# Performance work log

Measured on AMD Instinct MI355X. Metric: run time of the kernel, lower is better.

Reference implementation:

```python
import jax, jax.numpy as jnp
import numpy as np

# Grid / camera constants (from repo config and hardcoded module values)
D = 256                 # FRUSTUM3D.GRID_DIMENSIONS = [256,256,256]
TRUNC = 3.0             # FRUSTUM3D.TRUNCATION (densify default for geometry)
VOX = 0.03              # voxel size (points *= 0.03)
H, W = 240, 320         # rendered image size (from plot_image ticks)
FX = FY = 240.0
CX, CY = 160.0, 120.0
CENTER = jnp.array([3.825, 3.825, 3.825], dtype=jnp.float32)
OFFSETS = jnp.array([[0.0, 0.0, 0.0], [0.8, 0.0, 0.15], [0.75, 0.0, 0.1], [-0.85, 0.0, 0.1]], dtype=jnp.float32)
ANGLES = jnp.array([0.0, 0.0, 0.3, 2.15], dtype=jnp.float32)
N_PTS = 2_000_000


def setup_inputs() -> dict:
    key = jax.random.key(0)
    k1, k2, k3, k4 = jax.random.split(key, 4)
    # unique voxel coordinates (sparse tensor coords are unique by construction)
    flat = jax.random.permutation(k1, D * D * D)[:N_PTS]
    ix = flat // (D * D)
    iy = (flat // D) % D
    iz = flat % D
    geo_coords = jnp.stack([ix, iy, iz], axis=1).astype(jnp.int32)
    geo_feats = (jax.random.uniform(k2, (N_PTS,)) * 2.0).astype(jnp.float32)  # ~half < 1.0 -> surface
    rgb_feats = jax.random.uniform(k3, (N_PTS, 3), dtype=jnp.float32)
    aux_views = jax.random.uniform(k4, (1, 4, 3, H, W), dtype=jnp.float32)
    # valid SE(3) poses: identity rotation, camera at z = -6 looking toward the volume
    T = np.eye(4, dtype=np.float32)
    T[2, 3] = -6.0
    cam_poses = jnp.asarray(np.stack([T] * 4)[None])  # [1,4,4,4]
    return {"geo_coords": geo_coords, "geo_feats": geo_feats, "rgb_feats": rgb_feats,
            "aux_views": aux_views, "cam_poses": cam_poses}


def _rot_y(a):
    ca, sa = jnp.cos(a), jnp.sin(a)
    return jnp.array([[ca, 0.0, sa], [0.0, 1.0, 0.0], [-sa, 0.0, ca]], dtype=jnp.float32)


def reference(geo_coords, geo_feats, rgb_feats, aux_views, cam_poses):
    ix, iy, iz = geo_coords[:, 0], geo_coords[:, 1], geo_coords[:, 2]
    # sparse -> dense densify (geometry default = truncation, rgb default = 0)
    dense_geo = jnp.full((D, D, D), TRUNC, dtype=geo_feats.dtype).at[ix, iy, iz].set(geo_feats)
    dense_rgb = jnp.zeros((D, D, D, 3), dtype=rgb_feats.dtype).at[ix, iy, iz].set(rgb_feats)
    # surface extraction: geometry < 1.0 (non-set voxels have value TRUNC >= 1 -> never surface,
    # so surface voxels are exactly the input coords with feat < 1; fixed-shape masked form)
    surf = dense_geo[ix, iy, iz] < 1.0                      # [N]
    pts_rgb = dense_rgb[ix, iy, iz]                         # [N,3]  (= rgb[:, surface_mask].T)
    points = geo_coords.astype(jnp.float32) * VOX - CENTER  # [N,3]

    def render(T, offset, angle):
        R = T[:3, :3] @ _rot_y(angle)
        c = T[:3, 3] + offset
        pc = (points - c) @ R                               # camera-frame points, [N,3]
        z = pc[:, 2]
        vis = surf & (z > 1e-4)
        zs = jnp.where(vis, z, 1.0)
        u = jnp.round(FX * pc[:, 0] / zs + CX).astype(jnp.int32)
        v = jnp.round(FY * pc[:, 1] / zs + CY).astype(jnp.int32)
        inb = vis & (u >= 0) & (u < W) & (v >= 0) & (v < H)
        flat = jnp.where(inb, v * W + u, H * W)             # H*W -> dropped
        depth = jnp.where(inb, z, jnp.inf)
        zbuf = jnp.full(H * W, jnp.inf, dtype=jnp.float32).at[flat].min(depth, mode='drop')
        win = inb & (depth <= zbuf[jnp.clip(flat, 0, H * W - 1)])
        wf = win.astype(pts_rgb.dtype)
        num = jnp.zeros((H * W, 3), dtype=pts_rgb.dtype).at[flat].add(pts_rgb * wf[:, None], mode='drop')
        cnt = jnp.zeros((H * W,), dtype=pts_rgb.dtype).at[flat].add(wf, mode='drop')
        return (num / jnp.maximum(cnt, 1.0)[:, None]).reshape(H, W, 3)

    imgs = jax.vmap(render)(cam_poses[0], OFFSETS, ANGLES)          # [4,H,W,3]
    views = jnp.transpose(aux_views[0], (0, 2, 3, 1))               # [4,H,W,3]
    mask = (imgs != 0.0).astype(imgs.dtype)                         # elementwise, like torch.where(img==0,0,1)
    n = 3.0 * jnp.sum(mask, axis=(1, 2, 3))                         # per-view N
    l = jnp.sum(jnp.abs(imgs * mask - views * mask), axis=(1, 2, 3))
    return jnp.sum(jnp.where(n > 0, l / jnp.maximum(n, 1.0), 0.0))
```

## Files before the change

kernel.cpp:

```cpp
#include <hip/hip_runtime.h>

#define HWPIX (240 * 320)
#define VWORDS (4 * HWPIX)
#define NBINS 960
#define NB 256
#define CAP 3000000

__device__ __forceinline__ float dot3(float a0, float b0, float a1, float b1,
                                      float a2, float b2) {
  return __fadd_rn(__fadd_rn(__fmul_rn(a0, b0), __fmul_rn(a1, b1)),
                   __fmul_rn(a2, b2));
}

__device__ __forceinline__ bool project(const float* __restrict__ P, float px,
                                        float py, float pz, int& u, int& v,
                                        unsigned& zb) {
  float dx = __fsub_rn(px, P[9]);
  float dy = __fsub_rn(py, P[10]);
  float dz = __fsub_rn(pz, P[11]);
  float z = dot3(dx, P[2], dy, P[5], dz, P[8]);
  if (!(z > 1e-4f)) return false;
  float x = dot3(dx, P[0], dy, P[3], dz, P[6]);
  float y = dot3(dx, P[1], dy, P[4], dz, P[7]);
  u = (int)rintf(__fadd_rn(__fdiv_rn(__fmul_rn(240.0f, x), z), 160.0f));
  v = (int)rintf(__fadd_rn(__fdiv_rn(__fmul_rn(240.0f, y), z), 120.0f));
  if (u < 0 || u >= 320 || v < 0 || v >= 240) return false;
  zb = __float_as_uint(z);
  return true;
}

__global__ void k_init(const float* __restrict__ cam, float* __restrict__ params,
                       double* __restrict__ lacc, unsigned long long* __restrict__ macc) {
  int k = threadIdx.x;
  if (k >= 4) return;
  lacc[k] = 0.0;
  macc[k] = 0ull;
  const float offx[4] = {0.f, 0.8f, 0.75f, -0.85f};
  const float offy[4] = {0.f, 0.f, 0.f, 0.f};
  const float offz[4] = {0.f, 0.15f, 0.1f, 0.1f};
  const float angs[4] = {0.f, 0.f, 0.3f, 2.15f};
  const float* T = cam + k * 16;
  float ca = cosf(angs[k]);
  float sa = sinf(angs[k]);
  float Ry[3][3] = {{ca, 0.f, sa}, {0.f, 1.f, 0.f}, {-sa, 0.f, ca}};
  float* P = params + k * 16;
  for (int i = 0; i < 3; ++i)
    for (int j = 0; j < 3; ++j)
      P[i * 3 + j] = dot3(T[i * 4 + 0], Ry[0][j], T[i * 4 + 1], Ry[1][j],
                          T[i * 4 + 2], Ry[2][j]);
  P[9]  = __fadd_rn(T[3],  offx[k]);
  P[10] = __fadd_rn(T[7],  offy[k]);
  P[11] = __fadd_rn(T[11], offz[k]);
}

__global__ __launch_bounds__(1024) void k_count(const int* __restrict__ coords,
                                                const float* __restrict__ gfeat,
                                                const float* __restrict__ params,
                                                unsigned* __restrict__ hist, int N) {
  __shared__ unsigned h[NBINS];
  for (int j = threadIdx.x; j < NBINS; j += blockDim.x) h[j] = 0;
  __syncthreads();
  int chunk = (N + NB - 1) / NB;
  int lo = blockIdx.x * chunk, hi = min(N, lo + chunk);
  for (int i = lo + threadIdx.x; i < hi; i += blockDim.x) {
    if (!(gfeat[i] < 1.0f)) continue;
    float px = __fsub_rn(__fmul_rn((float)coords[3 * i + 0], 0.03f), 3.825f);
    float py = __fsub_rn(__fmul_rn((float)coords[3 * i + 1], 0.03f), 3.825f);
    float pz = __fsub_rn(__fmul_rn((float)coords[3 * i + 2], 0.03f), 3.825f);
#pragma unroll
    for (int k = 0; k < 4; ++k) {
      int u, v;
      unsigned zb;
      if (project(params + k * 16, px, py, pz, u, v, zb))
        atomicAdd(&h[k * 240 + v], 1u);
    }
  }
  __syncthreads();
  for (int j = threadIdx.x; j < NBINS; j += blockDim.x)
    hist[j * NB + blockIdx.x] = h[j];
}

__global__ __launch_bounds__(NB) void k_scan_bin(unsigned* __restrict__ hist,
                                                 unsigned* __restrict__ bin_tot) {
  __shared__ unsigned sc[NB];
  int b = blockIdx.x;
  int t = threadIdx.x;
  unsigned vin = hist[b * NB + t];
  sc[t] = vin;
  __syncthreads();
  for (int off = 1; off < NB; off <<= 1) {
    unsigned add = (t >= off) ? sc[t - off] : 0u;
    __syncthreads();
    sc[t] += add;
    __syncthreads();
  }
  hist[b * NB + t] = sc[t] - vin;
  if (t == NB - 1) bin_tot[b] = sc[t];
}

__global__ __launch_bounds__(1024) void k_scan_base(const unsigned* __restrict__ bin_tot,
                                                    unsigned* __restrict__ bin_base) {
  __shared__ unsigned sc[NBINS];
  int t = threadIdx.x;
  if (t < NBINS) sc[t] = bin_tot[t];
  __syncthreads();
  for (int off = 1; off < NBINS; off <<= 1) {
    unsigned add = (t < NBINS && t >= off) ? sc[t - off] : 0u;
    __syncthreads();
    if (t < NBINS) sc[t] += add;
    __syncthreads();
  }
  if (t < NBINS) bin_base[t] = sc[t] - bin_tot[t];
  if (t == 0) bin_base[NBINS] = sc[NBINS - 1];
}

__global__ __launch_bounds__(1024) void k_scatter(const int* __restrict__ coords,
                                                  const float* __restrict__ gfeat,
                                                  const float* __restrict__ params,
                                                  const unsigned* __restrict__ hist,
                                                  const unsigned* __restrict__ bin_base,
                                                  uint2* __restrict__ recs, int N) {
  __shared__ unsigned cur[NBINS];
  for (int j = threadIdx.x; j < NBINS; j += blockDim.x)
    cur[j] = bin_base[j] + hist[j * NB + blockIdx.x];
  __syncthreads();
  int chunk = (N + NB - 1) / NB;
  int lo = blockIdx.x * chunk, hi = min(N, lo + chunk);
  for (int i = lo + threadIdx.x; i < hi; i += blockDim.x) {
    if (!(gfeat[i] < 1.0f)) continue;
    float px = __fsub_rn(__fmul_rn((float)coords[3 * i + 0], 0.03f), 3.825f);
    float py = __fsub_rn(__fmul_rn((float)coords[3 * i + 1], 0.03f), 3.825f);
    float pz = __fsub_rn(__fmul_rn((float)coords[3 * i + 2], 0.03f), 3.825f);
#pragma unroll
    for (int k = 0; k < 4; ++k) {
      int u, v;
      unsigned zb;
      if (project(params + k * 16, px, py, pz, u, v, zb)) {
        unsigned slot = atomicAdd(&cur[k * 240 + v], 1u);
        if (slot < CAP)
          recs[slot] = make_uint2(zb, ((unsigned)i << 9) | (unsigned)u);
      }
    }
  }
}

__global__ __launch_bounds__(320) void k_render(const uint2* __restrict__ recs,
                                                const unsigned* __restrict__ bin_base,
                                                const float* __restrict__ rgb,
                                                const float* __restrict__ views,
                                                double* __restrict__ lacc,
                                                unsigned long long* __restrict__ macc) {
  int bin = blockIdx.x;
  int k = bin / 240, v = bin % 240;
  unsigned base = min(bin_base[bin], (unsigned)CAP);
  unsigned end = min(bin_base[bin + 1], (unsigned)CAP);
  if (end <= base) return;
  __shared__ unsigned zmin[320];
  __shared__ float num0[320], num1[320], num2[320], cnt[320];
  int t = threadIdx.x;
  zmin[t] = 0x7f800000u;
  num0[t] = num1[t] = num2[t] = cnt[t] = 0.f;
  __syncthreads();
  for (unsigned j = base + t; j < end; j += 320) {
    uint2 r = recs[j];
    atomicMin(&zmin[r.y & 511u], r.x);
  }
  __syncthreads();
  for (unsigned j = base + t; j < end; j += 320) {
    uint2 r = recs[j];
    unsigned u = r.y & 511u;
    if (r.x <= zmin[u]) {
      unsigned idx = r.y >> 9;
      atomicAdd(&num0[u], rgb[3 * idx + 0]);
      atomicAdd(&num1[u], rgb[3 * idx + 1]);
      atomicAdd(&num2[u], rgb[3 * idx + 2]);
      atomicAdd(&cnt[u], 1.0f);
    }
  }
  __syncthreads();
  float lsum = 0.f;
  unsigned mc = 0;
  {
    float denom = fmaxf(cnt[t], 1.0f);
    float i0 = __fdiv_rn(num0[t], denom);
    float i1 = __fdiv_rn(num1[t], denom);
    float i2 = __fdiv_rn(num2[t], denom);
    const float* vw = views + (size_t)(k * 3) * HWPIX + v * 320 + t;
    if (i0 != 0.f) { mc++; lsum += fabsf(__fsub_rn(i0, vw[0])); }
    if (i1 != 0.f) { mc++; lsum += fabsf(__fsub_rn(i1, vw[HWPIX])); }
    if (i2 != 0.f) { mc++; lsum += fabsf(__fsub_rn(i2, vw[2 * HWPIX])); }
  }
  for (int off = 32; off > 0; off >>= 1) {
    lsum += __shfl_down(lsum, off);
    mc += __shfl_down(mc, off);
  }
  __shared__ float sl[5];
  __shared__ unsigned sm[5];
  int lane = t & 63, wid = t >> 6;
  if (lane == 0) { sl[wid] = lsum; sm[wid] = mc; }
  __syncthreads();
  if (t == 0) {
    float L = 0.f;
    unsigned M = 0;
    for (int w = 0; w < 5; ++w) { L += sl[w]; M += sm[w]; }
    atomicAdd(&lacc[k], (double)L);
    atomicAdd(&macc[k], (unsigned long long)M);
  }
}

__global__ void k_final(const double* __restrict__ lacc,
                        const unsigned long long* __restrict__ macc,
                        float* __restrict__ out) {
  float total = 0.f;
  for (int k = 0; k < 4; ++k) {
    float n = 3.0f * (float)macc[k];
    float l = (float)lacc[k];
    if (n > 0.f) total += __fdiv_rn(l, fmaxf(n, 1.0f));
  }
  out[0] = total;
}

__global__ void kf_init(unsigned* __restrict__ zbuf, float* __restrict__ num,
                        float* __restrict__ cnt) {
  int i = blockIdx.x * blockDim.x + threadIdx.x;
  int stride = gridDim.x * blockDim.x;
  for (int j = i; j < VWORDS; j += stride) {
    zbuf[j] = 0x7f800000u;
    cnt[j] = 0.f;
  }
  for (int j = i; j < 3 * VWORDS; j += stride) num[j] = 0.f;
}

__global__ void kf_zmin(const int* __restrict__ coords, const float* __restrict__ gfeat,
                        const float* __restrict__ params, unsigned* __restrict__ zbuf,
                        int N) {
  int i = blockIdx.x * blockDim.x + threadIdx.x;
  if (i >= N) return;
  if (!(gfeat[i] < 1.0f)) return;
  float px = __fsub_rn(__fmul_rn((float)coords[3 * i + 0], 0.03f), 3.825f);
  float py = __fsub_rn(__fmul_rn((float)coords[3 * i + 1], 0.03f), 3.825f);
  float pz = __fsub_rn(__fmul_rn((float)coords[3 * i + 2], 0.03f), 3.825f);
#pragma unroll
  for (int k = 0; k < 4; ++k) {
    int u, v;
    unsigned zb;
    if (project(params + k * 16, px, py, pz, u, v, zb))
      atomicMin(&zbuf[k * HWPIX + v * 320 + u], zb);
  }
}

__global__ void kf_accum(const int* __restrict__ coords, const float* __restrict__ gfeat,
                         const float* __restrict__ rgb, const float* __restrict__ params,
                         const unsigned* __restrict__ zbuf, float* __restrict__ num,
                         float* __restrict__ cnt, int N) {
  int i = blockIdx.x * blockDim.x + threadIdx.x;
  if (i >= N) return;
  if (!(gfeat[i] < 1.0f)) return;
  float px = __fsub_rn(__fmul_rn((float)coords[3 * i + 0], 0.03f), 3.825f);
  float py = __fsub_rn(__fmul_rn((float)coords[3 * i + 1], 0.03f), 3.825f);
  float pz = __fsub_rn(__fmul_rn((float)coords[3 * i + 2], 0.03f), 3.825f);
#pragma unroll
  for (int k = 0; k < 4; ++k) {
    int u, v;
    unsigned zb;
    if (project(params + k * 16, px, py, pz, u, v, zb)) {
      int g = k * HWPIX + v * 320 + u;
      if (zb <= zbuf[g]) {
        atomicAdd(&num[g * 3 + 0], rgb[3 * i + 0]);
        atomicAdd(&num[g * 3 + 1], rgb[3 * i + 1]);
        atomicAdd(&num[g * 3 + 2], rgb[3 * i + 2]);
        atomicAdd(&cnt[g], 1.0f);
      }
    }
  }
}

__global__ void kf_loss(const float* __restrict__ num, const float* __restrict__ cnt,
                        const float* __restrict__ views, double* __restrict__ lacc,
                        unsigned long long* __restrict__ macc) {
  int k = blockIdx.y;
  int p = blockIdx.x * blockDim.x + threadIdx.x;
  float lsum = 0.f;
  unsigned mc = 0;
  if (p < HWPIX) {
    int fl = k * HWPIX + p;
    float denom = fmaxf(cnt[fl], 1.0f);
#pragma unroll
    for (int ch = 0; ch < 3; ++ch) {
      float img = __fdiv_rn(num[fl * 3 + ch], denom);
      if (img != 0.0f) {
        mc++;
        lsum += fabsf(__fsub_rn(img, views[(k * 3 + ch) * HWPIX + p]));
      }
    }
  }
  for (int off = 32; off > 0; off >>= 1) {
    lsum += __shfl_down(lsum, off);
    mc += __shfl_down(mc, off);
  }
  __shared__ float sl[4];
  __shared__ unsigned sm[4];
  int lane = threadIdx.x & 63, wid = threadIdx.x >> 6;
  if (lane == 0) { sl[wid] = lsum; sm[wid] = mc; }
  __syncthreads();
  if (threadIdx.x == 0) {
    atomicAdd(&lacc[k], (double)(sl[0] + sl[1] + sl[2] + sl[3]));
    atomicAdd(&macc[k], (unsigned long long)(sm[0] + sm[1] + sm[2] + sm[3]));
  }
}

extern "C" void kernel_launch(void* const* d_in, const int* in_sizes, int n_in,
                              void* d_out, int out_size, void* d_ws, size_t ws_size,
                              hipStream_t stream) {
  const int* coords = (const int*)d_in[0];
  const float* gfeat = (const float*)d_in[1];
  const float* rgb = (const float*)d_in[2];
  const float* views = (const float*)d_in[3];
  const float* cam = (const float*)d_in[4];
  int N = in_sizes[0] / 3;

  char* ws = (char*)d_ws;
  double* lacc = (double*)ws;
  unsigned long long* macc = (unsigned long long*)(ws + 32);
  float* params = (float*)(ws + 64);
  const size_t HDR = 512;

  const size_t HIST_B = (size_t)NBINS * NB * 4;
  const size_t TOT_B = (size_t)NBINS * 4;
  const size_t BASE_B = 4096;
  const size_t REC_B = (size_t)CAP * 8;
  const size_t need_fast = HDR + HIST_B + TOT_B + BASE_B + REC_B;

  if (ws_size >= need_fast) {
    unsigned* hist = (unsigned*)(ws + HDR);
    unsigned* bin_tot = (unsigned*)(ws + HDR + HIST_B);
    unsigned* bin_base = (unsigned*)(ws + HDR + HIST_B + TOT_B);
    uint2* recs = (uint2*)(ws + HDR + HIST_B + TOT_B + BASE_B);
    k_init<<<1, 64, 0, stream>>>(cam, params, lacc, macc);
    k_count<<<NB, 1024, 0, stream>>>(coords, gfeat, params, hist, N);
    k_scan_bin<<<NBINS, NB, 0, stream>>>(hist, bin_tot);
    k_scan_base<<<1, 1024, 0, stream>>>(bin_tot, bin_base);
    k_scatter<<<NB, 1024, 0, stream>>>(coords, gfeat, params, hist, bin_base, recs, N);
    k_render<<<NBINS, 320, 0, stream>>>(recs, bin_base, rgb, views, lacc, macc);
    k_final<<<1, 1, 0, stream>>>(lacc, macc, (float*)d_out);
  } else {
    unsigned* zbuf = (unsigned*)(ws + HDR);
    float* cnt = (float*)(ws + HDR + (size_t)VWORDS * 4);
    float* num = (float*)(ws + HDR + (size_t)VWORDS * 8);
    k_init<<<1, 64, 0, stream>>>(cam, params, lacc, macc);
    kf_init<<<1024, 256, 0, stream>>>(zbuf, num, cnt);
    int blocks = (N + 255) / 256;
    kf_zmin<<<blocks, 256, 0, stream>>>(coords, gfeat, params, zbuf, N);
    kf_accum<<<blocks, 256, 0, stream>>>(coords, gfeat, rgb, params, zbuf, num, cnt, N);
    kf_loss<<<dim3((HWPIX + 255) / 256, 4), 256, 0, stream>>>(num, cnt, views, lacc, macc);
    k_final<<<1, 1, 0, stream>>>(lacc, macc, (float*)d_out);
  }
}
```

Baseline: 82.46 us.

## Collapse pipeline into three kernels with fixed-capacity per-row bins

Replaces the seven-kernel count/scan/scatter/render/final pipeline with three kernels. Each block counts locally, reserves slots in fixed-size per-row bins with one global atomic per bin, then scatters records itself, so the separate scan kernels go away. The final reduction is folded into the render kernel through a last-block-done counter. This cuts launch count and the histogram scan passes, at the cost of recomputing the projections, needing a large workspace, and silently dropping records if a bin overflows maxper.

```diff
diff --git a/kernel.cpp b/kernel.cpp
--- a/kernel.cpp
+++ b/kernel.cpp
@@ -29,12 +29,8 @@
   return true;
 }
 
-__global__ void k_init(const float* __restrict__ cam, float* __restrict__ params,
-                       double* __restrict__ lacc, unsigned long long* __restrict__ macc) {
-  int k = threadIdx.x;
-  if (k >= 4) return;
-  lacc[k] = 0.0;
-  macc[k] = 0ull;
+__device__ __forceinline__ void compute_params(const float* __restrict__ cam,
+                                               float* __restrict__ params, int k) {
   const float offx[4] = {0.f, 0.8f, 0.75f, -0.85f};
   const float offy[4] = {0.f, 0.f, 0.f, 0.f};
   const float offz[4] = {0.f, 0.15f, 0.1f, 0.1f};
@@ -53,6 +49,166 @@
   P[11] = __fadd_rn(T[11], offz[k]);
 }
 
+
+__global__ __launch_bounds__(1024) void k_init3(const float* __restrict__ cam,
+                                                float* __restrict__ params,
+                                                double* __restrict__ lacc,
+                                                unsigned long long* __restrict__ macc,
+                                                unsigned* __restrict__ bin_cnt,
+                                                unsigned* __restrict__ done) {
+  int t = threadIdx.x;
+  if (t < 4) {
+    lacc[t] = 0.0;
+    macc[t] = 0ull;
+    compute_params(cam, params, t);
+  }
+  if (t == 4) *done = 0u;
+  if (t < NBINS) bin_cnt[t] = 0u;
+}
+
+__global__ __launch_bounds__(512) void k_build(const int* __restrict__ coords,
+                                               const float* __restrict__ gfeat,
+                                               const float* __restrict__ params,
+                                               unsigned* __restrict__ bin_cnt,
+                                               uint2* __restrict__ recs,
+                                               unsigned maxper, int N) {
+  __shared__ unsigned h[NBINS];
+  for (int j = threadIdx.x; j < NBINS; j += blockDim.x) h[j] = 0u;
+  __syncthreads();
+  int chunk = (N + gridDim.x - 1) / gridDim.x;
+  int lo = blockIdx.x * chunk, hi = min(N, lo + chunk);
+  for (int i = lo + threadIdx.x; i < hi; i += blockDim.x) {
+    if (!(gfeat[i] < 1.0f)) continue;
+    float px = __fsub_rn(__fmul_rn((float)coords[3 * i + 0], 0.03f), 3.825f);
+    float py = __fsub_rn(__fmul_rn((float)coords[3 * i + 1], 0.03f), 3.825f);
+    float pz = __fsub_rn(__fmul_rn((float)coords[3 * i + 2], 0.03f), 3.825f);
+#pragma unroll
+    for (int k = 0; k < 4; ++k) {
+      int u, v;
+      unsigned zb;
+      if (project(params + k * 16, px, py, pz, u, v, zb))
+        atomicAdd(&h[k * 240 + v], 1u);
+    }
+  }
+  __syncthreads();
+  for (int j = threadIdx.x; j < NBINS; j += blockDim.x) {
+    unsigned tot = h[j];
+    unsigned base = atomicAdd(&bin_cnt[j], tot);
+    h[j] = (unsigned)j * maxper + base;
+  }
+  __syncthreads();
+  for (int i = lo + threadIdx.x; i < hi; i += blockDim.x) {
+    if (!(gfeat[i] < 1.0f)) continue;
+    float px = __fsub_rn(__fmul_rn((float)coords[3 * i + 0], 0.03f), 3.825f);
+    float py = __fsub_rn(__fmul_rn((float)coords[3 * i + 1], 0.03f), 3.825f);
+    float pz = __fsub_rn(__fmul_rn((float)coords[3 * i + 2], 0.03f), 3.825f);
+#pragma unroll
+    for (int k = 0; k < 4; ++k) {
+      int u, v;
+      unsigned zb;
+      if (project(params + k * 16, px, py, pz, u, v, zb)) {
+        int bin = k * 240 + v;
+        unsigned slot = atomicAdd(&h[bin], 1u);
+        if (slot < (unsigned)(bin + 1) * maxper)
+          recs[slot] = make_uint2(zb, ((unsigned)i << 9) | (unsigned)u);
+      }
+    }
+  }
+}
+
+__global__ __launch_bounds__(320) void k_render3(const uint2* __restrict__ recs,
+                                                 const unsigned* __restrict__ bin_cnt,
+                                                 unsigned maxper,
+                                                 const float* __restrict__ rgb,
+                                                 const float* __restrict__ views,
+                                                 double* __restrict__ lacc,
+                                                 unsigned long long* __restrict__ macc,
+                                                 unsigned* __restrict__ done,
+                                                 float* __restrict__ out) {
+  int bin = blockIdx.x;
+  int k = bin / 240, v = bin % 240;
+  unsigned cnt_b = bin_cnt[bin];
+  if (cnt_b > maxper) cnt_b = maxper;
+  unsigned base = (unsigned)bin * maxper;
+  unsigned end = base + cnt_b;
+  int t = threadIdx.x;
+  if (cnt_b > 0) {
+    __shared__ unsigned zmin[320];
+    __shared__ float num0[320], num1[320], num2[320], cnt[320];
+    zmin[t] = 0x7f800000u;
+    num0[t] = num1[t] = num2[t] = cnt[t] = 0.f;
+    __syncthreads();
+    for (unsigned j = base + t; j < end; j += 320) {
+      uint2 r = recs[j];
+      atomicMin(&zmin[r.y & 511u], r.x);
+    }
+    __syncthreads();
+    for (unsigned j = base + t; j < end; j += 320) {
+      uint2 r = recs[j];
+      unsigned u = r.y & 511u;
+      if (r.x <= zmin[u]) {
+        unsigned idx = r.y >> 9;
+        atomicAdd(&num0[u], rgb[3 * idx + 0]);
+        atomicAdd(&num1[u], rgb[3 * idx + 1]);
+        atomicAdd(&num2[u], rgb[3 * idx + 2]);
+        atomicAdd(&cnt[u], 1.0f);
+      }
+    }
+    __syncthreads();
+    float lsum = 0.f;
+    unsigned mc = 0;
+    {
+      float denom = fmaxf(cnt[t], 1.0f);
+      float i0 = __fdiv_rn(num0[t], denom);
+      float i1 = __fdiv_rn(num1[t], denom);
+      float i2 = __fdiv_rn(num2[t], denom);
+      const float* vw = views + (size_t)(k * 3) * HWPIX + v * 320 + t;
+      if (i0 != 0.f) { mc++; lsum += fabsf(__fsub_rn(i0, vw[0])); }
+      if (i1 != 0.f) { mc++; lsum += fabsf(__fsub_rn(i1, vw[HWPIX])); }
+      if (i2 != 0.f) { mc++; lsum += fabsf(__fsub_rn(i2, vw[2 * HWPIX])); }
+    }
+    for (int off = 32; off > 0; off >>= 1) {
+      lsum += __shfl_down(lsum, off);
+      mc += __shfl_down(mc, off);
+    }
+    __shared__ float sl[5];
+    __shared__ unsigned sm[5];
+    int lane = t & 63, wid = t >> 6;
+    if (lane == 0) { sl[wid] = lsum; sm[wid] = mc; }
+    __syncthreads();
+    if (t == 0) {
+      float L = 0.f;
+      unsigned M = 0;
+      for (int w = 0; w < 5; ++w) { L += sl[w]; M += sm[w]; }
+      atomicAdd(&lacc[k], (double)L);
+      atomicAdd(&macc[k], (unsigned long long)M);
+    }
+  }
+  if (t == 0) {
+    __threadfence();
+    if (atomicAdd(done, 1u) == (unsigned)(NBINS - 1)) {
+      float total = 0.f;
+      for (int kk = 0; kk < 4; ++kk) {
+        double l = atomicAdd(&lacc[kk], 0.0);
+        unsigned long long m = atomicAdd(&macc[kk], 0ull);
+        float n = 3.0f * (float)m;
+        if (n > 0.f) total += __fdiv_rn((float)l, fmaxf(n, 1.0f));
+      }
+      out[0] = total;
+    }
+  }
+}
+
+
+__global__ void k_init(const float* __restrict__ cam, float* __restrict__ params,
+                       double* __restrict__ lacc, unsigned long long* __restrict__ macc) {
+  int k = threadIdx.x;
+  if (k >= 4) return;
+  lacc[k] = 0.0;
+  macc[k] = 0ull;
+  compute_params(cam, params, k);
+}
+
 __global__ __launch_bounds__(1024) void k_count(const int* __restrict__ coords,
                                                 const float* __restrict__ gfeat,
                                                 const float* __restrict__ params,
@@ -322,9 +478,25 @@
   char* ws = (char*)d_ws;
   double* lacc = (double*)ws;
   unsigned long long* macc = (unsigned long long*)(ws + 32);
-  float* params = (float*)(ws + 64);
-  const size_t HDR = 512;
-
+  unsigned* done = (unsigned*)(ws + 64);
+  float* params = (float*)(ws + 128);
+  unsigned* bin_cnt = (unsigned*)(ws + 512);
+  const size_t T1_HDR = 65536;
+
+  size_t maxper = 0;
+  if (ws_size > T1_HDR) maxper = (ws_size - T1_HDR) / ((size_t)NBINS * 8);
+  if (maxper > 131072) maxper = 131072;
+  if (maxper >= 30720) {
+    uint2* recs = (uint2*)(ws + T1_HDR);
+    k_init3<<<1, 1024, 0, stream>>>(cam, params, lacc, macc, bin_cnt, done);
+    k_build<<<512, 512, 0, stream>>>(coords, gfeat, params, bin_cnt, recs,
+                                     (unsigned)maxper, N);
+    k_render3<<<NBINS, 320, 0, stream>>>(recs, bin_cnt, (unsigned)maxper, rgb,
+                                         views, lacc, macc, done, (float*)d_out);
+    return;
+  }
+
+  const size_t HDR = 512 + 4096;
   const size_t HIST_B = (size_t)NBINS * NB * 4;
   const size_t TOT_B = (size_t)NBINS * 4;
   const size_t BASE_B = 4096;
```

After: 90.88 us. 10.2% more time.
